# Performance work log

Hardware: AMD Instinct MI355X
Metric: run time of the kernel (lower is better)

The kernel has to match this reference:

```python
import jax, jax.numpy as jnp
import numpy as np

N = 50000      # nodes
E = 800000     # edges (avg degree 16)
G = 1024       # graphs in batch
C = 128        # hidden / interaction channels
FIN = 16       # num_node_features
FE = 3         # num_edge_features
L = 3          # num_interactions
CUTOFF = 10.0
LOG2 = float(np.log(2.0))
BN_EPS = 1e-5

def ssp(v):
    # ShiftedSoftplus: softplus(x) - log(2)
    return jax.nn.softplus(v) - LOG2

def setup_inputs() -> dict:
    key = jax.random.key(0)
    ks = jax.random.split(key, 24)
    s = 0.05
    inp = {}
    inp["x"] = jax.random.normal(ks[0], (N, FIN), jnp.float32)
    inp["edge_index"] = jax.random.randint(ks[1], (2, E), 0, N, dtype=jnp.int32)
    inp["edge_weight"] = jax.random.uniform(ks[2], (E,), jnp.float32) * CUTOFF
    inp["edge_attr"] = jax.random.normal(ks[3], (E, FE), jnp.float32)
    inp["batch"] = jnp.sort(jax.random.randint(ks[4], (N,), 0, G, dtype=jnp.int32))
    # node embedding (node_data='x'): Linear(FIN,C) -> Linear(C,C)
    inp["W_l1"] = jax.random.normal(ks[5], (FIN, C), jnp.float32) * s
    inp["b_l1"] = jnp.zeros((C,), jnp.float32)
    inp["W_l2"] = jax.random.normal(ks[6], (C, C), jnp.float32) * s
    inp["b_l2"] = jnp.zeros((C,), jnp.float32)
    # BatchNorm1d affine params
    inp["bn_g"] = jnp.ones((C,), jnp.float32)
    inp["bn_b"] = jnp.zeros((C,), jnp.float32)
    # L stacked interaction layers (SchNet-style CFConv)
    inp["Wi_in"] = jax.random.normal(ks[7], (L, C, C), jnp.float32) * s
    inp["bi_in"] = jnp.zeros((L, C), jnp.float32)
    inp["We1"] = jax.random.normal(ks[8], (L, FE, C), jnp.float32) * s
    inp["be1"] = jnp.zeros((L, C), jnp.float32)
    inp["We2"] = jax.random.normal(ks[9], (L, C, C), jnp.float32) * s
    inp["be2"] = jnp.zeros((L, C), jnp.float32)
    inp["Wi_out"] = jax.random.normal(ks[10], (L, C, C), jnp.float32) * s
    inp["bi_out"] = jnp.zeros((L, C), jnp.float32)
    # GeneralReadOutLayer (128,'sum',32,1): pool -> Linear(128,32)+SSP -> Linear(32,1)+SSP
    inp["W_r1"] = jax.random.normal(ks[11], (C, 32), jnp.float32) * s
    inp["b_r1"] = jnp.zeros((32,), jnp.float32)
    inp["W_r2"] = jax.random.normal(ks[12], (32, 1), jnp.float32) * s
    inp["b_r2"] = jnp.zeros((1,), jnp.float32)
    return inp

def _forward(x, edge_weight, edge_attr,
             W_l1, b_l1, W_l2, b_l2, bn_g, bn_b,
             Wi_in, bi_in, We1, be1, We2, be2, Wi_out, bi_out,
             W_r1, b_r1, W_r2, b_r2, edge_index, batch):
    src, dst = edge_index[0], edge_index[1]
    # node embedding: Linear -> Linear
    h = (x @ W_l1 + b_l1) @ W_l2 + b_l2                   # [N, C]
    # BatchNorm1d (training-mode batch stats over nodes)
    mu = jnp.mean(h, axis=0)
    var = jnp.var(h, axis=0)
    h = (h - mu) * jax.lax.rsqrt(var + BN_EPS) * bn_g + bn_b
    # cosine cutoff envelope on edge distances
    env = 0.5 * (jnp.cos(edge_weight * (jnp.pi / CUTOFF)) + 1.0)  # [E]
    # GeoResNet: residual stack of interactions
    for i in range(L):
        filt = ssp(edge_attr @ We1[i] + be1[i]) @ We2[i] + be2[i]   # [E, C]
        hin = h @ Wi_in[i] + bi_in[i]                               # [N, C]
        msg = hin[src] * filt * env[:, None]                        # [E, C] gather
        agg = jax.ops.segment_sum(msg, dst, num_segments=N)         # [N, C] scatter
        h = h + ssp(agg @ Wi_out[i] + bi_out[i])
    # GeneralReadOutLayer: segment 'sum' pool then MLP with SSP
    hg = jax.ops.segment_sum(h, batch, num_segments=G)              # [G, C]
    out = ssp(hg @ W_r1 + b_r1)
    out = ssp(out @ W_r2 + b_r2)                                    # [G, 1]
    return out.reshape(-1)                                          # [G]

def reference(x, edge_index, edge_weight, edge_attr, batch,
              W_l1, b_l1, W_l2, b_l2, bn_g, bn_b,
              Wi_in, bi_in, We1, be1, We2, be2, Wi_out, bi_out,
              W_r1, b_r1, W_r2, b_r2):
    return _forward(x, edge_weight, edge_attr,
                    W_l1, b_l1, W_l2, b_l2, bn_g, bn_b,
                    Wi_in, bi_in, We1, be1, We2, be2, Wi_out, bi_out,
                    W_r1, b_r1, W_r2, b_r2, edge_index, batch)
```

## Files before the change

### kernel.cpp

```cpp
#include <hip/hip_runtime.h>
#include <hip/hip_bf16.h>
#include <math.h>

#define N_NODES 50000
#define N_EDGES 800000
#define N_GRAPH 1024
#define CDIM 128
#define FINDIM 16
#define NL 3
#define WTP 132

using short8  = __attribute__((ext_vector_type(8))) short;
using floatx4 = __attribute__((ext_vector_type(4))) float;

__device__ __forceinline__ float sspf(float x) {
    return __logf(1.0f + __expf(x)) - 0.6931471805599453f;
}

__device__ __forceinline__ unsigned short f2bf(float f) {
    unsigned int u = __float_as_uint(f);
    u = u + 0x7FFFu + ((u >> 16) & 1u);
    return (unsigned short)(u >> 16);
}

__device__ __forceinline__ float bf2f(unsigned short h) {
    return __uint_as_float((unsigned int)h << 16);
}

__device__ __forceinline__ unsigned int packbf(float a, float b) {
    __hip_bfloat162 h = __float22bfloat162_rn(make_float2(a, b));
    return *(unsigned int*)&h;
}

__device__ __forceinline__ short8 ldfrag(const unsigned short* T, int row, int k0) {
    const uint2* p = (const uint2*)(T + row * WTP + k0);
    short8 r;
    *(uint2*)&r       = p[0];
    *((uint2*)&r + 1) = p[1];
    return r;
}

__global__ void k_fuse(const float* __restrict__ Wl1, const float* __restrict__ bl1,
                       const float* __restrict__ Wl2, const float* __restrict__ bl2,
                       float* __restrict__ Wf, float* __restrict__ bfv) {
    int o = blockIdx.x * 256 + threadIdx.x;
    if (o < FINDIM * CDIM) {
        int f = o >> 7, c = o & 127;
        float s = 0.f;
#pragma unroll 4
        for (int k = 0; k < CDIM; ++k) s += Wl1[f * CDIM + k] * Wl2[k * CDIM + c];
        Wf[o] = s;
    } else if (o < FINDIM * CDIM + CDIM) {
        int c = o - FINDIM * CDIM;
        float s = bl2[c];
#pragma unroll 4
        for (int k = 0; k < CDIM; ++k) s += bl1[k] * Wl2[k * CDIM + c];
        bfv[c] = s;
    }
}

__global__ void k_embed_bn(const float* __restrict__ x, const float* __restrict__ Wf,
                           const float* __restrict__ bfv, float* __restrict__ h,
                           float* __restrict__ bnsum) {
    __shared__ float wfs[FINDIM * CDIM];
    __shared__ float bfs[CDIM];
    __shared__ float sd[512];
    for (int o = threadIdx.x; o < FINDIM * CDIM; o += 256) wfs[o] = Wf[o];
    if (threadIdx.x < CDIM) bfs[threadIdx.x] = bfv[threadIdx.x];
    __syncthreads();
    int c = threadIdx.x & 127;
    int half = threadIdx.x >> 7;
    float s1 = 0.f, s2 = 0.f;
    for (int base = blockIdx.x * 2; base < N_NODES; base += gridDim.x * 2) {
        int n = base + half;
        if (n < N_NODES) {
            float s = bfs[c];
            const float* xp = x + (size_t)n * FINDIM;
#pragma unroll
            for (int f = 0; f < FINDIM; ++f) s += xp[f] * wfs[f * CDIM + c];
            h[(size_t)n * CDIM + c] = s;
            s1 += s; s2 += s * s;
        }
    }
    sd[threadIdx.x] = s1; sd[256 + threadIdx.x] = s2;
    __syncthreads();
    if (threadIdx.x < 128) {
        atomicAdd(&bnsum[threadIdx.x], sd[threadIdx.x] + sd[threadIdx.x + 128]);
        atomicAdd(&bnsum[128 + threadIdx.x], sd[256 + threadIdx.x] + sd[256 + threadIdx.x + 128]);
    }
}

__global__ void k_bnapply(float* __restrict__ h, unsigned short* __restrict__ hb,
                          const float* __restrict__ bnsum,
                          const float* __restrict__ g, const float* __restrict__ b) {
    const float invN = 1.0f / (float)N_NODES;
    for (size_t i = (size_t)blockIdx.x * 256 + threadIdx.x; i < (size_t)N_NODES * CDIM;
         i += (size_t)gridDim.x * 256) {
        int c = (int)(i & 127);
        float mu  = bnsum[c] * invN;
        float var = bnsum[128 + c] * invN - mu * mu;
        float sc  = g[c] * rsqrtf(var + 1e-5f);
        float v = (h[i] - mu) * sc + b[c];
        h[i] = v;
        hb[i] = f2bf(v);
    }
}

__global__ void k_hist(const int* __restrict__ edst, int* __restrict__ deg) {
    int e = blockIdx.x * 256 + threadIdx.x;
    if (e < N_EDGES) atomicAdd(&deg[edst[e]], 1);
}

#define SCAN_T 1024
#define CHUNK 49
__global__ void k_scan(const int* __restrict__ deg, int* __restrict__ row_ptr) {
    __shared__ int part[SCAN_T];
    int t = threadIdx.x;
    int begin = t * CHUNK;
    int end   = begin + CHUNK; if (end > N_NODES) end = N_NODES;
    int s = 0;
    for (int i = begin; i < end && i < N_NODES; ++i) s += deg[i];
    part[t] = s;
    __syncthreads();
    for (int off = 1; off < SCAN_T; off <<= 1) {
        int v = (t >= off) ? part[t - off] : 0;
        __syncthreads();
        part[t] += v;
        __syncthreads();
    }
    int run = (t == 0) ? 0 : part[t - 1];
    for (int i = begin; i < end && i < N_NODES; ++i) { row_ptr[i] = run; run += deg[i]; }
    if (t == SCAN_T - 1) row_ptr[N_NODES] = run;
}

__global__ void k_scatter(const int* __restrict__ edst, const int* __restrict__ row_ptr,
                          int* __restrict__ cnt, int* __restrict__ perm) {
    int e = blockIdx.x * 256 + threadIdx.x;
    if (e < N_EDGES) {
        int d = edst[e];
        int pos = row_ptr[d] + atomicAdd(&cnt[d], 1);
        perm[pos] = e;
    }
}

__global__ void k_pack(const int* __restrict__ perm, const int* __restrict__ esrc,
                       const int* __restrict__ edst, const float* __restrict__ ew,
                       const float* __restrict__ ea,
                       int2* __restrict__ rmeta, float4* __restrict__ rea) {
    int i = blockIdx.x * 256 + threadIdx.x;
    if (i < N_EDGES) {
        int e = perm[i];
        float w = ew[e];
        float env = 0.5f * (__cosf(w * 0.31415926535897932f) + 1.0f);
        rmeta[i] = make_int2(esrc[e], edst[e]);
        rea[i] = make_float4(ea[(size_t)e * 3], ea[(size_t)e * 3 + 1], ea[(size_t)e * 3 + 2], env);
    }
}

__global__ __launch_bounds__(256, 2) void k_ngemm_in(const unsigned short* __restrict__ hb,
                                                     const float* __restrict__ B,
                                                     const float* __restrict__ bias,
                                                     unsigned short* __restrict__ hinb) {
    __shared__ unsigned short WT[128 * WTP];
    __shared__ float bs[CDIM];
    for (int o = threadIdx.x; o < CDIM * CDIM; o += 256) {
        int k = o >> 7, c = o & 127;
        WT[c * WTP + k] = f2bf(B[o]);
    }
    if (threadIdx.x < CDIM) bs[threadIdx.x] = bias[threadIdx.x];
    __syncthreads();

    int lane = threadIdx.x & 63, wave = threadIdx.x >> 6;
    int m = lane & 15, q = lane >> 4;
    int rb = blockIdx.x * 64 + wave * 16;
    int row = rb + m;
    if (row > N_NODES - 1) row = N_NODES - 1;

    floatx4 acc[8];
#pragma unroll
    for (int nt = 0; nt < 8; ++nt) acc[nt] = (floatx4){0.f, 0.f, 0.f, 0.f};

#pragma unroll
    for (int kb = 0; kb < 4; ++kb) {
        int k0 = kb * 32 + q * 8;
        short8 af = *(const short8*)(hb + (size_t)row * CDIM + k0);
#pragma unroll
        for (int nt = 0; nt < 8; ++nt) {
            short8 bf = ldfrag(WT, nt * 16 + m, k0);
            acc[nt] = __builtin_amdgcn_mfma_f32_16x16x32_bf16(af, bf, acc[nt], 0, 0, 0);
        }
    }
#pragma unroll
    for (int nt = 0; nt < 8; ++nt) {
        int c = nt * 16 + m;
#pragma unroll
        for (int r = 0; r < 4; ++r) {
            int orow = rb + q * 4 + r;
            if (orow < N_NODES)
                hinb[(size_t)orow * CDIM + c] = f2bf(acc[nt][r] + bs[c]);
        }
    }
}

__global__ __launch_bounds__(256, 2) void k_fused_oi(float* __restrict__ agg,
                                                     const float* __restrict__ Bo,
                                                     const float* __restrict__ bo,
                                                     float* __restrict__ h,
                                                     const float* __restrict__ Bi,
                                                     const float* __restrict__ bi,
                                                     unsigned short* __restrict__ hinb) {
    __shared__ unsigned short WT[128 * WTP];
    __shared__ unsigned short hnS[64 * WTP];
    __shared__ float bso[CDIM];
    __shared__ float bsi[CDIM];

    for (int o = threadIdx.x; o < CDIM * CDIM; o += 256) {
        int k = o >> 7, c = o & 127;
        WT[c * WTP + k] = f2bf(Bo[o]);
    }
    if (threadIdx.x < CDIM) { bso[threadIdx.x] = bo[threadIdx.x]; bsi[threadIdx.x] = bi[threadIdx.x]; }
    __syncthreads();

    int lane = threadIdx.x & 63, wave = threadIdx.x >> 6;
    int m = lane & 15, q = lane >> 4;
    int rb = blockIdx.x * 64 + wave * 16;
    int row = rb + m;
    if (row > N_NODES - 1) row = N_NODES - 1;

    floatx4 acc[8];
#pragma unroll
    for (int nt = 0; nt < 8; ++nt) acc[nt] = (floatx4){0.f, 0.f, 0.f, 0.f};

#pragma unroll
    for (int kb = 0; kb < 4; ++kb) {
        int k0 = kb * 32 + q * 8;
        const float* ap = agg + (size_t)row * CDIM + k0;
        float4 lo = *(const float4*)ap;
        float4 hi = *(const float4*)(ap + 4);
        short8 af;
        ((unsigned int*)&af)[0] = packbf(lo.x, lo.y);
        ((unsigned int*)&af)[1] = packbf(lo.z, lo.w);
        ((unsigned int*)&af)[2] = packbf(hi.x, hi.y);
        ((unsigned int*)&af)[3] = packbf(hi.z, hi.w);
#pragma unroll
        for (int nt = 0; nt < 8; ++nt) {
            short8 bf = ldfrag(WT, nt * 16 + m, k0);
            acc[nt] = __builtin_amdgcn_mfma_f32_16x16x32_bf16(af, bf, acc[nt], 0, 0, 0);
        }
    }

#pragma unroll
    for (int nt = 0; nt < 8; ++nt) {
        int c = nt * 16 + m;
#pragma unroll
        for (int r = 0; r < 4; ++r) {
            int lrow = wave * 16 + q * 4 + r;
            int orow = rb + q * 4 + r;
            if (orow < N_NODES) {
                size_t idx = (size_t)orow * CDIM + c;
                float hn = h[idx] + sspf(acc[nt][r] + bso[c]);
                h[idx] = hn;
                agg[idx] = 0.f;
                hnS[lrow * WTP + c] = f2bf(hn);
            } else {
                hnS[lrow * WTP + c] = 0;
            }
        }
    }
    __syncthreads();

    for (int o = threadIdx.x; o < CDIM * CDIM; o += 256) {
        int k = o >> 7, c = o & 127;
        WT[c * WTP + k] = f2bf(Bi[o]);
    }
    __syncthreads();

#pragma unroll
    for (int nt = 0; nt < 8; ++nt) acc[nt] = (floatx4){0.f, 0.f, 0.f, 0.f};
#pragma unroll
    for (int kb = 0; kb < 4; ++kb) {
        int k0 = kb * 32 + q * 8;
        short8 af = ldfrag(hnS, wave * 16 + m, k0);
#pragma unroll
        for (int nt = 0; nt < 8; ++nt) {
            short8 bf = ldfrag(WT, nt * 16 + m, k0);
            acc[nt] = __builtin_amdgcn_mfma_f32_16x16x32_bf16(af, bf, acc[nt], 0, 0, 0);
        }
    }
#pragma unroll
    for (int nt = 0; nt < 8; ++nt) {
        int c = nt * 16 + m;
#pragma unroll
        for (int r = 0; r < 4; ++r) {
            int orow = rb + q * 4 + r;
            if (orow < N_NODES)
                hinb[(size_t)orow * CDIM + c] = f2bf(acc[nt][r] + bsi[c]);
        }
    }
}

__global__ __launch_bounds__(256, 2) void k_ngemm_out_pool(const float* __restrict__ agg,
                                                           const float* __restrict__ B,
                                                           const float* __restrict__ bias,
                                                           const float* __restrict__ h,
                                                           const int* __restrict__ batch,
                                                           float* __restrict__ hg) {
    __shared__ unsigned short WT[128 * WTP];
    __shared__ float bs[CDIM];
    for (int o = threadIdx.x; o < CDIM * CDIM; o += 256) {
        int k = o >> 7, c = o & 127;
        WT[c * WTP + k] = f2bf(B[o]);
    }
    if (threadIdx.x < CDIM) bs[threadIdx.x] = bias[threadIdx.x];
    __syncthreads();

    int lane = threadIdx.x & 63, wave = threadIdx.x >> 6;
    int m = lane & 15, q = lane >> 4;
    int rb = blockIdx.x * 64 + wave * 16;
    int row = rb + m;
    if (row > N_NODES - 1) row = N_NODES - 1;

    floatx4 acc[8];
#pragma unroll
    for (int nt = 0; nt < 8; ++nt) acc[nt] = (floatx4){0.f, 0.f, 0.f, 0.f};

#pragma unroll
    for (int kb = 0; kb < 4; ++kb) {
        int k0 = kb * 32 + q * 8;
        const float* ap = agg + (size_t)row * CDIM + k0;
        float4 lo = *(const float4*)ap;
        float4 hi = *(const float4*)(ap + 4);
        short8 af;
        ((unsigned int*)&af)[0] = packbf(lo.x, lo.y);
        ((unsigned int*)&af)[1] = packbf(lo.z, lo.w);
        ((unsigned int*)&af)[2] = packbf(hi.x, hi.y);
        ((unsigned int*)&af)[3] = packbf(hi.z, hi.w);
#pragma unroll
        for (int nt = 0; nt < 8; ++nt) {
            short8 bf = ldfrag(WT, nt * 16 + m, k0);
            acc[nt] = __builtin_amdgcn_mfma_f32_16x16x32_bf16(af, bf, acc[nt], 0, 0, 0);
        }
    }

    int batchr[4];
#pragma unroll
    for (int r = 0; r < 4; ++r) {
        int orow = rb + q * 4 + r;
        batchr[r] = (orow < N_NODES) ? batch[orow] : 0;
    }
#pragma unroll
    for (int nt = 0; nt < 8; ++nt) {
        int c = nt * 16 + m;
#pragma unroll
        for (int r = 0; r < 4; ++r) {
            int orow = rb + q * 4 + r;
            if (orow < N_NODES) {
                size_t idx = (size_t)orow * CDIM + c;
                float hn = h[idx] + sspf(acc[nt][r] + bs[c]);
                atomicAdd(&hg[(size_t)batchr[r] * CDIM + c], hn);
            }
        }
    }
}

__global__ __launch_bounds__(256, 4) void k_edge(
    const float* __restrict__ We1, const float* __restrict__ be1,
    const float* __restrict__ We2, const float* __restrict__ be2,
    const int2* __restrict__ rmeta, const float4* __restrict__ rea,
    const unsigned short* __restrict__ hin, float* __restrict__ agg) {
    __shared__ unsigned short WT[128 * WTP];
    __shared__ float4 we1i[CDIM];
    __shared__ float  be2s[CDIM];
    __shared__ int2   sds[64];
    __shared__ float4 eas4[64];

    for (int o = threadIdx.x; o < CDIM * CDIM; o += 256) {
        int k = o >> 7, c = o & 127;
        WT[c * WTP + k] = f2bf(We2[o]);
    }
    if (threadIdx.x < CDIM) {
        int k = threadIdx.x;
        we1i[k] = make_float4(We1[k], We1[CDIM + k], We1[2 * CDIM + k], be1[k]);
        be2s[k] = be2[k];
    }
    __syncthreads();

    int lane = threadIdx.x & 63, wave = threadIdx.x >> 6;
    int m = lane & 15, q = lane >> 4;

    float biasr[8];
#pragma unroll
    for (int nt = 0; nt < 8; ++nt) biasr[nt] = be2s[nt * 16 + m];

    const int ntiles = N_EDGES / 64;
    int tpb = (ntiles + gridDim.x - 1) / gridDim.x;
    int t0 = blockIdx.x * tpb;
    int t1 = t0 + tpb; if (t1 > ntiles) t1 = ntiles;

    for (int tile = t0; tile < t1; ++tile) {
        int s0 = tile * 64;
        __syncthreads();
        if (threadIdx.x < 64)       sds[threadIdx.x]       = rmeta[s0 + threadIdx.x];
        else if (threadIdx.x < 128) eas4[threadIdx.x - 64] = rea[s0 + threadIdx.x - 64];
        __syncthreads();

        int el0 = wave * 16 + q * 4;
        int2 sd[4]; float ev[4];
#pragma unroll
        for (int r = 0; r < 4; ++r) { sd[r] = sds[el0 + r]; ev[r] = eas4[el0 + r].w; }

        unsigned short hpre[4][8];
#pragma unroll
        for (int r = 0; r < 4; ++r) {
            const unsigned short* hp = hin + (size_t)sd[r].x * CDIM + m;
#pragma unroll
            for (int nt = 0; nt < 8; ++nt) hpre[r][nt] = hp[nt * 16];
        }

        float4 eav = eas4[wave * 16 + m];
        float ea0 = eav.x, ea1 = eav.y, ea2 = eav.z;
        short8 af[4];
#pragma unroll
        for (int kb = 0; kb < 4; ++kb) {
#pragma unroll
            for (int jj = 0; jj < 4; ++jj) {
                int k = kb * 32 + q * 8 + jj * 2;
                float4 w0 = we1i[k];
                float4 w1 = we1i[k + 1];
                float p0 = fmaf(w0.x, ea0, fmaf(w0.y, ea1, fmaf(w0.z, ea2, w0.w)));
                float p1 = fmaf(w1.x, ea0, fmaf(w1.y, ea1, fmaf(w1.z, ea2, w1.w)));
                ((unsigned int*)&af[kb])[jj] = packbf(sspf(p0), sspf(p1));
            }
        }

        floatx4 acc[8];
#pragma unroll
        for (int nt = 0; nt < 8; ++nt)
            acc[nt] = (floatx4){biasr[nt], biasr[nt], biasr[nt], biasr[nt]};
#pragma unroll
        for (int kb = 0; kb < 4; ++kb)
#pragma unroll
            for (int nt = 0; nt < 8; ++nt) {
                short8 bf = ldfrag(WT, nt * 16 + m, kb * 32 + q * 8);
                acc[nt] = __builtin_amdgcn_mfma_f32_16x16x32_bf16(af[kb], bf, acc[nt], 0, 0, 0);
            }

        bool uni = (sd[0].y == sd[3].y);
        float vv[8];
#pragma unroll
        for (int nt = 0; nt < 8; ++nt) {
            float s = 0.f;
#pragma unroll
            for (int r = 0; r < 4; ++r)
                s += acc[nt][r] * ev[r] * bf2f(hpre[r][nt]);
            vv[nt] = s;
        }

        int owner = uni ? 1 : 0;
        int myd   = uni ? sd[0].y : -1 - lane;
#pragma unroll
        for (int s = 16; s <= 32; s <<= 1) {
            int od = __shfl_xor(myd, s, 64);
            int oo = __shfl_xor(owner, s, 64);
            bool match = owner && oo && (od == myd);
            bool lower = ((lane & s) == 0);
#pragma unroll
            for (int nt = 0; nt < 8; ++nt) {
                float ovv = __shfl_xor(vv[nt], s, 64);
                if (match && lower) vv[nt] += ovv;
            }
            if (match && !lower) { owner = 0; myd = -1 - lane; }
        }

        if (uni) {
            if (owner) {
                float* ap = agg + (size_t)myd * CDIM + m;
#pragma unroll
                for (int nt = 0; nt < 8; ++nt) atomicAdd(&ap[nt * 16], vv[nt]);
            }
        } else {
#pragma unroll
            for (int nt = 0; nt < 8; ++nt) {
                int c = nt * 16 + m;
                int cur = sd[0].y;
                float accv = acc[nt][0] * ev[0] * bf2f(hpre[0][nt]);
#pragma unroll
                for (int r = 1; r < 4; ++r) {
                    float msg = acc[nt][r] * ev[r] * bf2f(hpre[r][nt]);
                    if (sd[r].y != cur) {
                        atomicAdd(&agg[(size_t)cur * CDIM + c], accv);
                        cur = sd[r].y; accv = msg;
                    } else {
                        accv += msg;
                    }
                }
                atomicAdd(&agg[(size_t)cur * CDIM + c], accv);
            }
        }
    }
}

__global__ void k_readout(const float* __restrict__ hg, const float* __restrict__ Wr1,
                          const float* __restrict__ br1, const float* __restrict__ Wr2,
                          const float* __restrict__ br2, float* __restrict__ out) {
    __shared__ float hgs[CDIM];
    int g = blockIdx.x;
    for (int o = threadIdx.x; o < CDIM; o += 64) hgs[o] = hg[(size_t)g * CDIM + o];
    __syncthreads();
    int c = threadIdx.x;
    float val = 0.f;
    if (c < 32) {
        float s = br1[c];
        for (int k = 0; k < CDIM; ++k) s += hgs[k] * Wr1[k * 32 + c];
        val = sspf(s) * Wr2[c];
    }
#pragma unroll
    for (int off = 16; off >= 1; off >>= 1) val += __shfl_down(val, off, 32);
    if (c == 0) out[g] = sspf(val + br2[0]);
}

extern "C" void kernel_launch(void* const* d_in, const int* in_sizes, int n_in,
                              void* d_out, int out_size, void* d_ws, size_t ws_size,
                              hipStream_t stream) {
    const float* x     = (const float*)d_in[0];
    const int*   eidx  = (const int*)  d_in[1];
    const float* ew    = (const float*)d_in[2];
    const float* ea    = (const float*)d_in[3];
    const int*   batch = (const int*)  d_in[4];
    const float* Wl1   = (const float*)d_in[5];
    const float* bl1   = (const float*)d_in[6];
    const float* Wl2   = (const float*)d_in[7];
    const float* bl2   = (const float*)d_in[8];
    const float* bng   = (const float*)d_in[9];
    const float* bnb   = (const float*)d_in[10];
    const float* Wi_in = (const float*)d_in[11];
    const float* bi_in = (const float*)d_in[12];
    const float* We1   = (const float*)d_in[13];
    const float* be1   = (const float*)d_in[14];
    const float* We2   = (const float*)d_in[15];
    const float* be2   = (const float*)d_in[16];
    const float* Wi_o  = (const float*)d_in[17];
    const float* bi_o  = (const float*)d_in[18];
    const float* Wr1   = (const float*)d_in[19];
    const float* br1   = (const float*)d_in[20];
    const float* Wr2   = (const float*)d_in[21];
    const float* br2   = (const float*)d_in[22];
    float* out = (float*)d_out;

    float* ws  = (float*)d_ws;
    float*  h    = ws;
    float*  agg  = h + (size_t)N_NODES * CDIM;
    float4* rea  = (float4*)(agg + (size_t)N_NODES * CDIM);
    float*  hg   = (float*)(rea + N_EDGES);
    float*  Wf   = hg + (size_t)N_GRAPH * CDIM;
    float*  bfv  = Wf + FINDIM * CDIM;
    float*  bnsum = bfv + CDIM;
    unsigned short* hb   = (unsigned short*)(bnsum + 256);
    unsigned short* hinb = hb + (size_t)N_NODES * CDIM;
    int2*  rmeta  = (int2*)(hinb + (size_t)N_NODES * CDIM);
    int*   perm   = (int*)(rmeta + N_EDGES);
    int*   deg    = perm + N_EDGES;
    int*   row_ptr= deg + N_NODES;
    int*   cnt    = row_ptr + N_NODES + 1;

    const int* esrc = eidx;
    const int* edst = eidx + N_EDGES;

    hipMemsetAsync(deg, 0, (size_t)N_NODES * sizeof(int), stream);
    hipMemsetAsync(cnt, 0, (size_t)N_NODES * sizeof(int), stream);
    k_hist<<<(N_EDGES + 255) / 256, 256, 0, stream>>>(edst, deg);
    k_scan<<<1, SCAN_T, 0, stream>>>(deg, row_ptr);
    k_scatter<<<(N_EDGES + 255) / 256, 256, 0, stream>>>(edst, row_ptr, cnt, perm);
    k_pack<<<(N_EDGES + 255) / 256, 256, 0, stream>>>(perm, esrc, edst, ew, ea, rmeta, rea);

    hipMemsetAsync(bnsum, 0, 256 * sizeof(float), stream);
    k_fuse<<<9, 256, 0, stream>>>(Wl1, bl1, Wl2, bl2, Wf, bfv);
    k_embed_bn<<<512, 256, 0, stream>>>(x, Wf, bfv, h, bnsum);
    k_bnapply<<<1024, 256, 0, stream>>>(h, hb, bnsum, bng, bnb);

    hipMemsetAsync(agg, 0, (size_t)N_NODES * CDIM * sizeof(float), stream);
    hipMemsetAsync(hg, 0, (size_t)N_GRAPH * CDIM * sizeof(float), stream);
    const int ngrid = (N_NODES + 63) / 64;

    k_ngemm_in<<<ngrid, 256, 0, stream>>>(hb, Wi_in, bi_in, hinb);
    for (int l = 0; l < NL; ++l) {
        k_edge<<<1024, 256, 0, stream>>>(We1 + l * 3 * CDIM, be1 + l * CDIM,
                                         We2 + (size_t)l * CDIM * CDIM, be2 + l * CDIM,
                                         rmeta, rea, hinb, agg);
        if (l < NL - 1)
            k_fused_oi<<<ngrid, 256, 0, stream>>>(agg, Wi_o + (size_t)l * CDIM * CDIM,
                                                  bi_o + l * CDIM, h,
                                                  Wi_in + (size_t)(l + 1) * CDIM * CDIM,
                                                  bi_in + (l + 1) * CDIM, hinb);
        else
            k_ngemm_out_pool<<<ngrid, 256, 0, stream>>>(agg, Wi_o + (size_t)l * CDIM * CDIM,
                                                        bi_o + l * CDIM, h, batch, hg);
    }

    k_readout<<<N_GRAPH, 64, 0, stream>>>(hg, Wr1, br1, Wr2, br2, out);
}
```

Measured before the change: 985.7 us.

## Parallelize CSR scan, fuse scatter with pack, fold BN apply into first GEMM

Replaces the single-block serial degree scan with a three-kernel multi-block scan. It fuses edge scatter and packing so the perm buffer and one pass over the edges disappear. BatchNorm application is folded into the first input GEMM: the kernel normalizes h on load, writes it back, and packs it to bf16. This removes a full elementwise pass and the hb buffer. In exchange there are extra launches, and the scatter writes become random when packing edge data.

```diff
diff --git a/kernel.cpp b/kernel.cpp
--- a/kernel.cpp
+++ b/kernel.cpp
@@ -9,6 +9,7 @@
 #define FINDIM 16
 #define NL 3
 #define WTP 132
+#define NSCB 196
 
 using short8  = __attribute__((ext_vector_type(8))) short;
 using floatx4 = __attribute__((ext_vector_type(4))) float;
@@ -90,91 +91,105 @@
     }
 }
 
-__global__ void k_bnapply(float* __restrict__ h, unsigned short* __restrict__ hb,
-                          const float* __restrict__ bnsum,
-                          const float* __restrict__ g, const float* __restrict__ b) {
-    const float invN = 1.0f / (float)N_NODES;
-    for (size_t i = (size_t)blockIdx.x * 256 + threadIdx.x; i < (size_t)N_NODES * CDIM;
-         i += (size_t)gridDim.x * 256) {
-        int c = (int)(i & 127);
-        float mu  = bnsum[c] * invN;
-        float var = bnsum[128 + c] * invN - mu * mu;
-        float sc  = g[c] * rsqrtf(var + 1e-5f);
-        float v = (h[i] - mu) * sc + b[c];
-        h[i] = v;
-        hb[i] = f2bf(v);
-    }
-}
-
 __global__ void k_hist(const int* __restrict__ edst, int* __restrict__ deg) {
     int e = blockIdx.x * 256 + threadIdx.x;
     if (e < N_EDGES) atomicAdd(&deg[edst[e]], 1);
 }
 
-#define SCAN_T 1024
-#define CHUNK 49
-__global__ void k_scan(const int* __restrict__ deg, int* __restrict__ row_ptr) {
-    __shared__ int part[SCAN_T];
+__global__ void k_scan1(const int* __restrict__ deg, int* __restrict__ bsum) {
+    __shared__ int sd[256];
+    int i = blockIdx.x * 256 + threadIdx.x;
+    sd[threadIdx.x] = (i < N_NODES) ? deg[i] : 0;
+    __syncthreads();
+    for (int off = 128; off > 0; off >>= 1) {
+        if (threadIdx.x < off) sd[threadIdx.x] += sd[threadIdx.x + off];
+        __syncthreads();
+    }
+    if (threadIdx.x == 0) bsum[blockIdx.x] = sd[0];
+}
+
+__global__ void k_scan2(const int* __restrict__ bsum, int* __restrict__ boff,
+                        int* __restrict__ row_ptr) {
+    __shared__ int sd[256];
     int t = threadIdx.x;
-    int begin = t * CHUNK;
-    int end   = begin + CHUNK; if (end > N_NODES) end = N_NODES;
-    int s = 0;
-    for (int i = begin; i < end && i < N_NODES; ++i) s += deg[i];
-    part[t] = s;
-    __syncthreads();
-    for (int off = 1; off < SCAN_T; off <<= 1) {
-        int v = (t >= off) ? part[t - off] : 0;
+    int v = (t < NSCB) ? bsum[t] : 0;
+    sd[t] = v;
+    __syncthreads();
+    for (int off = 1; off < 256; off <<= 1) {
+        int u = (t >= off) ? sd[t - off] : 0;
         __syncthreads();
-        part[t] += v;
+        sd[t] += u;
         __syncthreads();
     }
-    int run = (t == 0) ? 0 : part[t - 1];
-    for (int i = begin; i < end && i < N_NODES; ++i) { row_ptr[i] = run; run += deg[i]; }
-    if (t == SCAN_T - 1) row_ptr[N_NODES] = run;
-}
-
-__global__ void k_scatter(const int* __restrict__ edst, const int* __restrict__ row_ptr,
-                          int* __restrict__ cnt, int* __restrict__ perm) {
+    if (t < NSCB) boff[t] = sd[t] - v;
+    if (t == 255) row_ptr[N_NODES] = sd[255];
+}
+
+__global__ void k_scan3(const int* __restrict__ deg, const int* __restrict__ boff,
+                        int* __restrict__ row_ptr) {
+    __shared__ int sd[256];
+    int i = blockIdx.x * 256 + threadIdx.x;
+    int t = threadIdx.x;
+    int v = (i < N_NODES) ? deg[i] : 0;
+    sd[t] = v;
+    __syncthreads();
+    for (int off = 1; off < 256; off <<= 1) {
+        int u = (t >= off) ? sd[t - off] : 0;
+        __syncthreads();
+        sd[t] += u;
+        __syncthreads();
+    }
+    if (i < N_NODES) row_ptr[i] = boff[blockIdx.x] + sd[t] - v;
+}
+
+__global__ void k_scatter_pack(const int* __restrict__ esrc, const int* __restrict__ edst,
+                               const float* __restrict__ ew, const float* __restrict__ ea,
+                               const int* __restrict__ row_ptr, int* __restrict__ cnt,
+                               int2* __restrict__ rmeta, float4* __restrict__ rea) {
     int e = blockIdx.x * 256 + threadIdx.x;
     if (e < N_EDGES) {
         int d = edst[e];
         int pos = row_ptr[d] + atomicAdd(&cnt[d], 1);
-        perm[pos] = e;
-    }
-}
-
-__global__ void k_pack(const int* __restrict__ perm, const int* __restrict__ esrc,
-                       const int* __restrict__ edst, const float* __restrict__ ew,
-                       const float* __restrict__ ea,
-                       int2* __restrict__ rmeta, float4* __restrict__ rea) {
-    int i = blockIdx.x * 256 + threadIdx.x;
-    if (i < N_EDGES) {
-        int e = perm[i];
+        rmeta[pos] = make_int2(esrc[e], d);
         float w = ew[e];
         float env = 0.5f * (__cosf(w * 0.31415926535897932f) + 1.0f);
-        rmeta[i] = make_int2(esrc[e], edst[e]);
-        rea[i] = make_float4(ea[(size_t)e * 3], ea[(size_t)e * 3 + 1], ea[(size_t)e * 3 + 2], env);
-    }
-}
-
-__global__ __launch_bounds__(256, 2) void k_ngemm_in(const unsigned short* __restrict__ hb,
-                                                     const float* __restrict__ B,
-                                                     const float* __restrict__ bias,
-                                                     unsigned short* __restrict__ hinb) {
+        rea[pos] = make_float4(ea[(size_t)e * 3], ea[(size_t)e * 3 + 1],
+                               ea[(size_t)e * 3 + 2], env);
+    }
+}
+
+__global__ __launch_bounds__(256, 2) void k_ngemm_in_bn(float* __restrict__ h,
+                                                        const float* __restrict__ bnsum,
+                                                        const float* __restrict__ g,
+                                                        const float* __restrict__ b,
+                                                        const float* __restrict__ B,
+                                                        const float* __restrict__ bias,
+                                                        unsigned short* __restrict__ hinb) {
     __shared__ unsigned short WT[128 * WTP];
     __shared__ float bs[CDIM];
+    __shared__ float scale[CDIM];
+    __shared__ float shift[CDIM];
     for (int o = threadIdx.x; o < CDIM * CDIM; o += 256) {
         int k = o >> 7, c = o & 127;
         WT[c * WTP + k] = f2bf(B[o]);
     }
-    if (threadIdx.x < CDIM) bs[threadIdx.x] = bias[threadIdx.x];
+    if (threadIdx.x < CDIM) {
+        int c = threadIdx.x;
+        const float invN = 1.0f / (float)N_NODES;
+        float mu  = bnsum[c] * invN;
+        float var = bnsum[128 + c] * invN - mu * mu;
+        float sc  = g[c] * rsqrtf(var + 1e-5f);
+        scale[c] = sc;
+        shift[c] = b[c] - mu * sc;
+        bs[c] = bias[c];
+    }
     __syncthreads();
 
     int lane = threadIdx.x & 63, wave = threadIdx.x >> 6;
     int m = lane & 15, q = lane >> 4;
     int rb = blockIdx.x * 64 + wave * 16;
-    int row = rb + m;
-    if (row > N_NODES - 1) row = N_NODES - 1;
+    bool rowok = (rb + m) < N_NODES;
+    int row = rowok ? (rb + m) : (N_NODES - 1);
 
     floatx4 acc[8];
 #pragma unroll
@@ -183,7 +198,23 @@
 #pragma unroll
     for (int kb = 0; kb < 4; ++kb) {
         int k0 = kb * 32 + q * 8;
-        short8 af = *(const short8*)(hb + (size_t)row * CDIM + k0);
+        float* ap = h + (size_t)row * CDIM + k0;
+        float4 lo = *(const float4*)ap;
+        float4 hi = *(const float4*)(ap + 4);
+        lo.x = fmaf(lo.x, scale[k0 + 0], shift[k0 + 0]);
+        lo.y = fmaf(lo.y, scale[k0 + 1], shift[k0 + 1]);
+        lo.z = fmaf(lo.z, scale[k0 + 2], shift[k0 + 2]);
+        lo.w = fmaf(lo.w, scale[k0 + 3], shift[k0 + 3]);
+        hi.x = fmaf(hi.x, scale[k0 + 4], shift[k0 + 4]);
+        hi.y = fmaf(hi.y, scale[k0 + 5], shift[k0 + 5]);
+        hi.z = fmaf(hi.z, scale[k0 + 6], shift[k0 + 6]);
+        hi.w = fmaf(hi.w, scale[k0 + 7], shift[k0 + 7]);
+        if (rowok) { *(float4*)ap = lo; *(float4*)(ap + 4) = hi; }
+        short8 af;
+        ((unsigned int*)&af)[0] = packbf(lo.x, lo.y);
+        ((unsigned int*)&af)[1] = packbf(lo.z, lo.w);
+        ((unsigned int*)&af)[2] = packbf(hi.x, hi.y);
+        ((unsigned int*)&af)[3] = packbf(hi.z, hi.w);
 #pragma unroll
         for (int nt = 0; nt < 8; ++nt) {
             short8 bf = ldfrag(WT, nt * 16 + m, k0);
@@ -555,13 +586,13 @@
     float*  Wf   = hg + (size_t)N_GRAPH * CDIM;
     float*  bfv  = Wf + FINDIM * CDIM;
     float*  bnsum = bfv + CDIM;
-    unsigned short* hb   = (unsigned short*)(bnsum + 256);
-    unsigned short* hinb = hb + (size_t)N_NODES * CDIM;
+    unsigned short* hinb = (unsigned short*)(bnsum + 256);
     int2*  rmeta  = (int2*)(hinb + (size_t)N_NODES * CDIM);
-    int*   perm   = (int*)(rmeta + N_EDGES);
-    int*   deg    = perm + N_EDGES;
+    int*   deg    = (int*)(rmeta + N_EDGES);
     int*   row_ptr= deg + N_NODES;
     int*   cnt    = row_ptr + N_NODES + 1;
+    int*   bsum   = cnt + N_NODES;
+    int*   boff   = bsum + NSCB;
 
     const int* esrc = eidx;
     const int* edst = eidx + N_EDGES;
@@ -569,20 +600,21 @@
     hipMemsetAsync(deg, 0, (size_t)N_NODES * sizeof(int), stream);
     hipMemsetAsync(cnt, 0, (size_t)N_NODES * sizeof(int), stream);
     k_hist<<<(N_EDGES + 255) / 256, 256, 0, stream>>>(edst, deg);
-    k_scan<<<1, SCAN_T, 0, stream>>>(deg, row_ptr);
-    k_scatter<<<(N_EDGES + 255) / 256, 256, 0, stream>>>(edst, row_ptr, cnt, perm);
-    k_pack<<<(N_EDGES + 255) / 256, 256, 0, stream>>>(perm, esrc, edst, ew, ea, rmeta, rea);
+    k_scan1<<<NSCB, 256, 0, stream>>>(deg, bsum);
+    k_scan2<<<1, 256, 0, stream>>>(bsum, boff, row_ptr);
+    k_scan3<<<NSCB, 256, 0, stream>>>(deg, boff, row_ptr);
+    k_scatter_pack<<<(N_EDGES + 255) / 256, 256, 0, stream>>>(esrc, edst, ew, ea,
+                                                              row_ptr, cnt, rmeta, rea);
 
     hipMemsetAsync(bnsum, 0, 256 * sizeof(float), stream);
     k_fuse<<<9, 256, 0, stream>>>(Wl1, bl1, Wl2, bl2, Wf, bfv);
     k_embed_bn<<<512, 256, 0, stream>>>(x, Wf, bfv, h, bnsum);
-    k_bnapply<<<1024, 256, 0, stream>>>(h, hb, bnsum, bng, bnb);
 
     hipMemsetAsync(agg, 0, (size_t)N_NODES * CDIM * sizeof(float), stream);
     hipMemsetAsync(hg, 0, (size_t)N_GRAPH * CDIM * sizeof(float), stream);
     const int ngrid = (N_NODES + 63) / 64;
 
-    k_ngemm_in<<<ngrid, 256, 0, stream>>>(hb, Wi_in, bi_in, hinb);
+    k_ngemm_in_bn<<<ngrid, 256, 0, stream>>>(h, bnsum, bng, bnb, Wi_in, bi_in, hinb);
     for (int l = 0; l < NL; ++l) {
         k_edge<<<1024, 256, 0, stream>>>(We1 + l * 3 * CDIM, be1 + l * CDIM,
                                          We2 + (size_t)l * CDIM * CDIM, be2 + l * CDIM,
```

Measured after the change: 861.4 us. -12.6%, faster.
